# Performance work log

Hardware: AMD Instinct MI355X
Metric: run time of the kernel (lower is better)

Reference implementation:

```python
import jax, jax.numpy as jnp
import numpy as np

D_IN = 256
H = 512


def _linear_params(key, fan_in, fan_out):
    kw, kb = jax.random.split(key)
    bound = 1.0 / np.sqrt(fan_in)
    W = jax.random.uniform(kw, (fan_in, fan_out), minval=-bound, maxval=bound, dtype=jnp.float32)
    b = jax.random.uniform(kb, (fan_out,), minval=-bound, maxval=bound, dtype=jnp.float32)
    return W, b


def setup_inputs() -> dict:
    key = jax.random.key(0)
    ks = jax.random.split(key, 7)
    brick_vectors = jax.random.normal(ks[0], (8, 128, D_IN), dtype=jnp.float32)
    Wa, ba = _linear_params(ks[1], D_IN, H)
    Wb, bb = _linear_params(ks[2], H, H)
    Wca, bca = _linear_params(ks[3], 2 * H, H)
    Wcb, bcb = _linear_params(ks[4], H, H)
    Wcc, bcc = _linear_params(ks[5], H, H)
    Wo, bo = _linear_params(ks[6], H, 2)
    return {
        "brick_vectors": brick_vectors,
        "Wa": Wa, "ba": ba,
        "Wb": Wb, "bb": bb,
        "Wca": Wca, "bca": bca,
        "Wcb": Wcb, "bcb": bcb,
        "Wcc": Wcc, "bcc": bcc,
        "Wo": Wo, "bo": bo,
    }


def reference(brick_vectors, Wa, ba, Wb, bb, Wca, bca, Wcb, bcb, Wcc, bcc, Wo, bo):
    B, N, _ = brick_vectors.shape
    x = brick_vectors.reshape(-1, D_IN)            # [B*N, D_IN]
    f = jax.nn.relu(x @ Wa + ba)                   # node MLP
    f = jax.nn.relu(f @ Wb + bb)                   # [B*N, 512]
    f = f.reshape(B, N, H)
    # pairwise broadcast-concat: pair (i, j) gets cat(f[:, j], f[:, i])
    fa = jnp.broadcast_to(f[:, None, :, :], (B, N, N, H))   # varies over j (last pair axis)
    fb = jnp.broadcast_to(f[:, :, None, :], (B, N, N, H))   # varies over i
    e = jnp.concatenate((fa, fb), axis=-1).reshape(-1, 2 * H)  # [B*N*N, 1024]
    e = jax.nn.relu(e @ Wca + bca)
    e = jax.nn.relu(e @ Wcb + bcb)
    e = jax.nn.relu(e @ Wcc + bcc)
    out = e @ Wo + bo                               # [B*N*N, 2]
    return out.reshape(B, N, N, 2)
```

## Files before the change

kernel.cpp:

```cpp
#include <hip/hip_runtime.h>

typedef __bf16 bf16x8 __attribute__((ext_vector_type(8)));
typedef float f32x16 __attribute__((ext_vector_type(16)));

__global__ __launch_bounds__(256) void prep_pack(const float* __restrict__ Wcb,
                                                 const float* __restrict__ Wcc,
                                                 __bf16* __restrict__ Pb,
                                                 __bf16* __restrict__ Pc) {
  int idx = blockIdx.x * 256 + threadIdx.x;
  const float* src = (idx < 262144) ? Wcb : Wcc;
  __bf16* dst = (idx < 262144) ? Pb : Pc;
  int t = idx & 262143;
  int e = t & 7, l = (t >> 3) & 63, kb = (t >> 9) & 31, c = t >> 14;
  int k = kb * 16 + ((l >> 5) << 3) + e;
  int n = (c << 5) + (l & 31);
  dst[t] = (__bf16)src[k * 512 + n];
}

__global__ __launch_bounds__(256) void gemm_f32(const float* __restrict__ A,
                                                const float* __restrict__ W,
                                                const float* __restrict__ bias,
                                                float* __restrict__ C,
                                                int K, int N, int do_relu) {
  __shared__ float As[16][68];
  __shared__ float Ws[16][32];
  int bm = blockIdx.x * 64, bn = blockIdx.y * 32;
  int tid = threadIdx.x;
  int tx = tid & 15, ty = tid >> 4;
  float acc[4][2] = {};
  for (int k0 = 0; k0 < K; k0 += 16) {
#pragma unroll
    for (int ii = 0; ii < 4; ii++) {
      int e = ii * 256 + tid; int r = e >> 4, c = e & 15;
      As[c][r] = A[(bm + r) * K + k0 + c];
    }
#pragma unroll
    for (int ii = 0; ii < 2; ii++) {
      int e = ii * 256 + tid; int kr = e >> 5, c = e & 31;
      Ws[kr][c] = W[(k0 + kr) * N + bn + c];
    }
    __syncthreads();
#pragma unroll
    for (int kk = 0; kk < 16; kk++) {
      float4 a = *(const float4*)&As[kk][ty * 4];
      float2 w = *(const float2*)&Ws[kk][tx * 2];
      acc[0][0] += a.x * w.x; acc[0][1] += a.x * w.y;
      acc[1][0] += a.y * w.x; acc[1][1] += a.y * w.y;
      acc[2][0] += a.z * w.x; acc[2][1] += a.z * w.y;
      acc[3][0] += a.w * w.x; acc[3][1] += a.w * w.y;
    }
    __syncthreads();
  }
#pragma unroll
  for (int mi = 0; mi < 4; mi++)
#pragma unroll
    for (int ni = 0; ni < 2; ni++) {
      int n = bn + tx * 2 + ni;
      float vv = acc[mi][ni] + (bias ? bias[n] : 0.f);
      if (do_relu) vv = fmaxf(vv, 0.f);
      C[(bm + ty * 4 + mi) * N + n] = vv;
    }
}

__global__ __launch_bounds__(256) void gemm_uv(const float* __restrict__ A,
                                               const float* __restrict__ Wca,
                                               float* __restrict__ u,
                                               float* __restrict__ v) {
  __shared__ float As[16][68];
  __shared__ float Ws[16][32];
  int half = blockIdx.y >> 4;
  const float* W = Wca + half * 512 * 512;
  float* C = half ? v : u;
  int bm = blockIdx.x * 64, bn = (blockIdx.y & 15) * 32;
  int tid = threadIdx.x;
  int tx = tid & 15, ty = tid >> 4;
  float acc[4][2] = {};
  for (int k0 = 0; k0 < 512; k0 += 16) {
#pragma unroll
    for (int ii = 0; ii < 4; ii++) {
      int e = ii * 256 + tid; int r = e >> 4, c = e & 15;
      As[c][r] = A[(bm + r) * 512 + k0 + c];
    }
#pragma unroll
    for (int ii = 0; ii < 2; ii++) {
      int e = ii * 256 + tid; int kr = e >> 5, c = e & 31;
      Ws[kr][c] = W[(k0 + kr) * 512 + bn + c];
    }
    __syncthreads();
#pragma unroll
    for (int kk = 0; kk < 16; kk++) {
      float4 a = *(const float4*)&As[kk][ty * 4];
      float2 w = *(const float2*)&Ws[kk][tx * 2];
      acc[0][0] += a.x * w.x; acc[0][1] += a.x * w.y;
      acc[1][0] += a.y * w.x; acc[1][1] += a.y * w.y;
      acc[2][0] += a.z * w.x; acc[2][1] += a.z * w.y;
      acc[3][0] += a.w * w.x; acc[3][1] += a.w * w.y;
    }
    __syncthreads();
  }
#pragma unroll
  for (int mi = 0; mi < 4; mi++)
#pragma unroll
    for (int ni = 0; ni < 2; ni++)
      C[(bm + ty * 4 + mi) * 512 + bn + tx * 2 + ni] = acc[mi][ni];
}

__global__ __launch_bounds__(512, 2) void edge_kernel(
    const float* __restrict__ u, const float* __restrict__ v,
    const bf16x8* __restrict__ Pb, const bf16x8* __restrict__ Pc,
    const float* __restrict__ bca, const float* __restrict__ bcb,
    const float* __restrict__ bcc, const float* __restrict__ Wo,
    const float* __restrict__ bo, float* __restrict__ out) {
  __shared__ __align__(16) char h_raw[131072];

  int wg = blockIdx.x;
  int i = wg & 127, b = wg >> 7;
  int tid = threadIdx.x, lane = tid & 63, w = tid >> 6;

  int mrow = (w & 1) * 32;
  int n0 = (w >> 1) * 128;
  int cg4 = (w >> 1) * 4;
  int arow = mrow + (lane & 31);
  int sA = (arow & 15) << 4;
  int klo = (lane >> 5) * 8;

  const bf16x8* Bb0 = Pb + ((cg4 + 0) * 32) * 64 + lane;
  const bf16x8* Bb1 = Pb + ((cg4 + 1) * 32) * 64 + lane;
  const bf16x8* Bb2 = Pb + ((cg4 + 2) * 32) * 64 + lane;
  const bf16x8* Bb3 = Pb + ((cg4 + 3) * 32) * 64 + lane;
  const bf16x8* Bc0 = Pc + ((cg4 + 0) * 32) * 64 + lane;
  const bf16x8* Bc1 = Pc + ((cg4 + 1) * 32) * 64 + lane;
  const bf16x8* Bc2 = Pc + ((cg4 + 2) * 32) * 64 + lane;
  const bf16x8* Bc3 = Pc + ((cg4 + 3) * 32) * 64 + lane;

  bf16x8 pf0 = Bb0[0], pf1 = Bb1[0], pf2 = Bb2[0], pf3 = Bb3[0];

  {
    int k2 = tid & 255;
    float2 vv = *(const float2*)(v + (b * 128 + i) * 512 + 2 * k2);
    float2 bc = *(const float2*)(bca + 2 * k2);
    float vb0 = vv.x + bc.x, vb1 = vv.y + bc.y;
    const float* ub = u + (b * 128) * 512;
#pragma unroll 4
    for (int it = 0; it < 64; it++) {
      int r = it * 2 + (tid >> 8);
      float2 uu = *(const float2*)(ub + r * 512 + 2 * k2);
      float x0 = fmaxf(uu.x + vb0, 0.f);
      float x1 = fmaxf(uu.y + vb1, 0.f);
      unsigned short s0 = __builtin_bit_cast(unsigned short, (__bf16)x0);
      unsigned short s1 = __builtin_bit_cast(unsigned short, (__bf16)x1);
      unsigned int pk = ((unsigned int)s1 << 16) | (unsigned int)s0;
      int rt = r & 63;
      int wbyte = ((r >> 6) << 16) + rt * 1024 + ((4 * k2) ^ ((rt & 15) << 4));
      *(unsigned int*)(h_raw + wbyte) = pk;
    }
  }
  __syncthreads();

  f32x16 acc0[4], acc1[4];

#pragma unroll
  for (int nb = 0; nb < 4; nb++)
#pragma unroll
    for (int r = 0; r < 16; r++) { acc0[nb][r] = 0.f; acc1[nb][r] = 0.f; }
#pragma unroll 2
  for (int kb = 0; kb < 32; kb++) {
    bf16x8 b0 = pf0, b1 = pf1, b2 = pf2, b3 = pf3;
    if (kb < 31) {
      pf0 = Bb0[(kb + 1) * 64];
      pf1 = Bb1[(kb + 1) * 64];
      pf2 = Bb2[(kb + 1) * 64];
      pf3 = Bb3[(kb + 1) * 64];
    }
    int abyte = arow * 1024 + (((kb * 16 + klo) * 2) ^ sA);
    bf16x8 a0 = *(const bf16x8*)(h_raw + abyte);
    bf16x8 a1 = *(const bf16x8*)(h_raw + 65536 + abyte);
    acc0[0] = __builtin_amdgcn_mfma_f32_32x32x16_bf16(a0, b0, acc0[0], 0, 0, 0);
    acc1[0] = __builtin_amdgcn_mfma_f32_32x32x16_bf16(a1, b0, acc1[0], 0, 0, 0);
    acc0[1] = __builtin_amdgcn_mfma_f32_32x32x16_bf16(a0, b1, acc0[1], 0, 0, 0);
    acc1[1] = __builtin_amdgcn_mfma_f32_32x32x16_bf16(a1, b1, acc1[1], 0, 0, 0);
    acc0[2] = __builtin_amdgcn_mfma_f32_32x32x16_bf16(a0, b2, acc0[2], 0, 0, 0);
    acc1[2] = __builtin_amdgcn_mfma_f32_32x32x16_bf16(a1, b2, acc1[2], 0, 0, 0);
    acc0[3] = __builtin_amdgcn_mfma_f32_32x32x16_bf16(a0, b3, acc0[3], 0, 0, 0);
    acc1[3] = __builtin_amdgcn_mfma_f32_32x32x16_bf16(a1, b3, acc1[3], 0, 0, 0);
  }

  pf0 = Bc0[0]; pf1 = Bc1[0]; pf2 = Bc2[0]; pf3 = Bc3[0];
  __syncthreads();

#pragma unroll
  for (int nb = 0; nb < 4; nb++) {
    int cn = n0 + nb * 32 + (lane & 31);
    float bbv = bcb[cn];
#pragma unroll
    for (int r = 0; r < 16; r++) {
      int row = mrow + (r & 3) + 8 * (r >> 2) + 4 * (lane >> 5);
      int byte_ = row * 1024 + ((cn * 2) ^ ((row & 15) << 4));
      *(__bf16*)(h_raw + byte_) = (__bf16)fmaxf(acc0[nb][r] + bbv, 0.f);
      *(__bf16*)(h_raw + 65536 + byte_) = (__bf16)fmaxf(acc1[nb][r] + bbv, 0.f);
    }
  }
  __syncthreads();

#pragma unroll
  for (int nb = 0; nb < 4; nb++)
#pragma unroll
    for (int r = 0; r < 16; r++) { acc0[nb][r] = 0.f; acc1[nb][r] = 0.f; }
#pragma unroll 2
  for (int kb = 0; kb < 32; kb++) {
    bf16x8 b0 = pf0, b1 = pf1, b2 = pf2, b3 = pf3;
    if (kb < 31) {
      pf0 = Bc0[(kb + 1) * 64];
      pf1 = Bc1[(kb + 1) * 64];
      pf2 = Bc2[(kb + 1) * 64];
      pf3 = Bc3[(kb + 1) * 64];
    }
    int abyte = arow * 1024 + (((kb * 16 + klo) * 2) ^ sA);
    bf16x8 a0 = *(const bf16x8*)(h_raw + abyte);
    bf16x8 a1 = *(const bf16x8*)(h_raw + 65536 + abyte);
    acc0[0] = __builtin_amdgcn_mfma_f32_32x32x16_bf16(a0, b0, acc0[0], 0, 0, 0);
    acc1[0] = __builtin_amdgcn_mfma_f32_32x32x16_bf16(a1, b0, acc1[0], 0, 0, 0);
    acc0[1] = __builtin_amdgcn_mfma_f32_32x32x16_bf16(a0, b1, acc0[1], 0, 0, 0);
    acc1[1] = __builtin_amdgcn_mfma_f32_32x32x16_bf16(a1, b1, acc1[1], 0, 0, 0);
    acc0[2] = __builtin_amdgcn_mfma_f32_32x32x16_bf16(a0, b2, acc0[2], 0, 0, 0);
    acc1[2] = __builtin_amdgcn_mfma_f32_32x32x16_bf16(a1, b2, acc1[2], 0, 0, 0);
    acc0[3] = __builtin_amdgcn_mfma_f32_32x32x16_bf16(a0, b3, acc0[3], 0, 0, 0);
    acc1[3] = __builtin_amdgcn_mfma_f32_32x32x16_bf16(a1, b3, acc1[3], 0, 0, 0);
  }

  float p0[16][2] = {}, p1[16][2] = {};
#pragma unroll
  for (int nb = 0; nb < 4; nb++) {
    int cn = n0 + nb * 32 + (lane & 31);
    float bcv = bcc[cn];
    float2 wov = *(const float2*)(Wo + cn * 2);
#pragma unroll
    for (int r = 0; r < 16; r++) {
      float h30 = fmaxf(acc0[nb][r] + bcv, 0.f);
      float h31 = fmaxf(acc1[nb][r] + bcv, 0.f);
      p0[r][0] += h30 * wov.x; p0[r][1] += h30 * wov.y;
      p1[r][0] += h31 * wov.x; p1[r][1] += h31 * wov.y;
    }
  }
#pragma unroll
  for (int m = 1; m <= 16; m <<= 1) {
#pragma unroll
    for (int r = 0; r < 16; r++) {
      p0[r][0] += __shfl_xor(p0[r][0], m, 64);
      p0[r][1] += __shfl_xor(p0[r][1], m, 64);
      p1[r][0] += __shfl_xor(p1[r][0], m, 64);
      p1[r][1] += __shfl_xor(p1[r][1], m, 64);
    }
  }
  __syncthreads();
  float* red = (float*)h_raw;
  if ((lane & 31) == 0) {
    int hh = lane >> 5, cg = w >> 1;
#pragma unroll
    for (int r = 0; r < 16; r++) {
      int row = mrow + (r & 3) + 8 * (r >> 2) + 4 * hh;
      red[(cg * 128 + row) * 2 + 0] = p0[r][0];
      red[(cg * 128 + row) * 2 + 1] = p0[r][1];
      red[(cg * 128 + 64 + row) * 2 + 0] = p1[r][0];
      red[(cg * 128 + 64 + row) * 2 + 1] = p1[r][1];
    }
  }
  __syncthreads();
  if (tid < 256) {
    int row = tid >> 1, d = tid & 1;
    float s = red[(0 * 128 + row) * 2 + d] + red[(1 * 128 + row) * 2 + d] +
              red[(2 * 128 + row) * 2 + d] + red[(3 * 128 + row) * 2 + d] + bo[d];
    out[((b * 128 + i) * 128 + row) * 2 + d] = s;
  }
}

extern "C" void kernel_launch(void* const* d_in, const int* in_sizes, int n_in,
                              void* d_out, int out_size, void* d_ws, size_t ws_size,
                              hipStream_t stream) {
  const float* x   = (const float*)d_in[0];
  const float* Wa  = (const float*)d_in[1];
  const float* ba  = (const float*)d_in[2];
  const float* Wb  = (const float*)d_in[3];
  const float* bb  = (const float*)d_in[4];
  const float* Wca = (const float*)d_in[5];
  const float* bca = (const float*)d_in[6];
  const float* Wcb = (const float*)d_in[7];
  const float* bcb = (const float*)d_in[8];
  const float* Wcc = (const float*)d_in[9];
  const float* bcc = (const float*)d_in[10];
  const float* Wo  = (const float*)d_in[11];
  const float* bo  = (const float*)d_in[12];
  float* out = (float*)d_out;

  char* ws = (char*)d_ws;
  float* f1 = (float*)(ws);
  float* f  = (float*)(ws + (2u << 20));
  float* u  = (float*)(ws + (4u << 20));
  float* v  = (float*)(ws + (6u << 20));
  __bf16* Pb = (__bf16*)(ws + (8u << 20));
  __bf16* Pc = (__bf16*)(ws + (8u << 20) + (512u << 10));

  prep_pack<<<2048, 256, 0, stream>>>(Wcb, Wcc, Pb, Pc);
  gemm_f32<<<dim3(16, 16), 256, 0, stream>>>(x, Wa, ba, f1, 256, 512, 1);
  gemm_f32<<<dim3(16, 16), 256, 0, stream>>>(f1, Wb, bb, f, 512, 512, 1);
  gemm_uv<<<dim3(16, 32), 256, 0, stream>>>(f, Wca, u, v);
  edge_kernel<<<1024, 512, 0, stream>>>(u, v, (const bf16x8*)Pb, (const bf16x8*)Pc,
                                        bca, bcb, bcc, Wo, bo, out);
}
```

Before: 255.6 us.

## Stage packed weight tiles into LDS with double-buffered global_load_lds

Previously every wave loaded its own B fragments for the two edge-MLP GEMMs straight from global memory into registers. Wave pairs with different row halves loaded identical data, so each fragment was fetched twice. The new code has each wave fetch two column-blocks of the next k-slice directly into a double-buffered LDS region through the global-to-LDS load path. All waves then read their four fragments from LDS. This removes the duplicated global traffic and the register prefetch, but adds a workgroup barrier on every k-iteration and grows the LDS allocation to 160 KB.

```diff
diff --git a/kernel.cpp b/kernel.cpp
--- a/kernel.cpp
+++ b/kernel.cpp
@@ -2,6 +2,11 @@
 
 typedef __bf16 bf16x8 __attribute__((ext_vector_type(8)));
 typedef float f32x16 __attribute__((ext_vector_type(16)));
+
+#define GLOAD_LDS16(gsrc, ldst)                                                   \
+  __builtin_amdgcn_global_load_lds(                                               \
+      (const __attribute__((address_space(1))) void*)(gsrc),                      \
+      (__attribute__((address_space(3))) void*)(ldst), 16, 0, 0)
 
 __global__ __launch_bounds__(256) void prep_pack(const float* __restrict__ Wcb,
                                                  const float* __restrict__ Wcc,
@@ -111,7 +116,8 @@
     const float* __restrict__ bca, const float* __restrict__ bcb,
     const float* __restrict__ bcc, const float* __restrict__ Wo,
     const float* __restrict__ bo, float* __restrict__ out) {
-  __shared__ __align__(16) char h_raw[131072];
+  __shared__ __align__(16) char h_raw[163840];
+  char* Bst = h_raw + 131072;
 
   int wg = blockIdx.x;
   int i = wg & 127, b = wg >> 7;
@@ -123,17 +129,17 @@
   int arow = mrow + (lane & 31);
   int sA = (arow & 15) << 4;
   int klo = (lane >> 5) * 8;
-
-  const bf16x8* Bb0 = Pb + ((cg4 + 0) * 32) * 64 + lane;
-  const bf16x8* Bb1 = Pb + ((cg4 + 1) * 32) * 64 + lane;
-  const bf16x8* Bb2 = Pb + ((cg4 + 2) * 32) * 64 + lane;
-  const bf16x8* Bb3 = Pb + ((cg4 + 3) * 32) * 64 + lane;
-  const bf16x8* Bc0 = Pc + ((cg4 + 0) * 32) * 64 + lane;
-  const bf16x8* Bc1 = Pc + ((cg4 + 1) * 32) * 64 + lane;
-  const bf16x8* Bc2 = Pc + ((cg4 + 2) * 32) * 64 + lane;
-  const bf16x8* Bc3 = Pc + ((cg4 + 3) * 32) * 64 + lane;
-
-  bf16x8 pf0 = Bb0[0], pf1 = Bb1[0], pf2 = Bb2[0], pf3 = Bb3[0];
+  int cb0 = 2 * w;
+
+#define STAGE_B(P, kb, sel)                                                       \
+  {                                                                               \
+    const char* _g0 = (const char*)((P) + (cb0 * 32 + (kb)) * 64) + lane * 16;    \
+    const char* _g1 = (const char*)((P) + ((cb0 + 1) * 32 + (kb)) * 64) + lane * 16; \
+    GLOAD_LDS16(_g0, Bst + (sel) * 16384 + cb0 * 1024);                           \
+    GLOAD_LDS16(_g1, Bst + (sel) * 16384 + (cb0 + 1) * 1024);                     \
+  }
+
+  STAGE_B(Pb, 0, 0)
 
   {
     int k2 = tid & 255;
@@ -165,13 +171,13 @@
     for (int r = 0; r < 16; r++) { acc0[nb][r] = 0.f; acc1[nb][r] = 0.f; }
 #pragma unroll 2
   for (int kb = 0; kb < 32; kb++) {
-    bf16x8 b0 = pf0, b1 = pf1, b2 = pf2, b3 = pf3;
-    if (kb < 31) {
-      pf0 = Bb0[(kb + 1) * 64];
-      pf1 = Bb1[(kb + 1) * 64];
-      pf2 = Bb2[(kb + 1) * 64];
-      pf3 = Bb3[(kb + 1) * 64];
-    }
+    int sel = kb & 1;
+    if (kb < 31) STAGE_B(Pb, kb + 1, sel ^ 1)
+    const char* bb = Bst + sel * 16384 + lane * 16;
+    bf16x8 b0 = *(const bf16x8*)(bb + (cg4 + 0) * 1024);
+    bf16x8 b1 = *(const bf16x8*)(bb + (cg4 + 1) * 1024);
+    bf16x8 b2 = *(const bf16x8*)(bb + (cg4 + 2) * 1024);
+    bf16x8 b3 = *(const bf16x8*)(bb + (cg4 + 3) * 1024);
     int abyte = arow * 1024 + (((kb * 16 + klo) * 2) ^ sA);
     bf16x8 a0 = *(const bf16x8*)(h_raw + abyte);
     bf16x8 a1 = *(const bf16x8*)(h_raw + 65536 + abyte);
@@ -183,10 +189,9 @@
     acc1[2] = __builtin_amdgcn_mfma_f32_32x32x16_bf16(a1, b2, acc1[2], 0, 0, 0);
     acc0[3] = __builtin_amdgcn_mfma_f32_32x32x16_bf16(a0, b3, acc0[3], 0, 0, 0);
     acc1[3] = __builtin_amdgcn_mfma_f32_32x32x16_bf16(a1, b3, acc1[3], 0, 0, 0);
-  }
-
-  pf0 = Bc0[0]; pf1 = Bc1[0]; pf2 = Bc2[0]; pf3 = Bc3[0];
-  __syncthreads();
+    __syncthreads();
+  }
+  STAGE_B(Pc, 0, 0)
 
 #pragma unroll
   for (int nb = 0; nb < 4; nb++) {
@@ -208,13 +213,13 @@
     for (int r = 0; r < 16; r++) { acc0[nb][r] = 0.f; acc1[nb][r] = 0.f; }
 #pragma unroll 2
   for (int kb = 0; kb < 32; kb++) {
-    bf16x8 b0 = pf0, b1 = pf1, b2 = pf2, b3 = pf3;
-    if (kb < 31) {
-      pf0 = Bc0[(kb + 1) * 64];
-      pf1 = Bc1[(kb + 1) * 64];
-      pf2 = Bc2[(kb + 1) * 64];
-      pf3 = Bc3[(kb + 1) * 64];
-    }
+    int sel = kb & 1;
+    if (kb < 31) STAGE_B(Pc, kb + 1, sel ^ 1)
+    const char* bb = Bst + sel * 16384 + lane * 16;
+    bf16x8 b0 = *(const bf16x8*)(bb + (cg4 + 0) * 1024);
+    bf16x8 b1 = *(const bf16x8*)(bb + (cg4 + 1) * 1024);
+    bf16x8 b2 = *(const bf16x8*)(bb + (cg4 + 2) * 1024);
+    bf16x8 b3 = *(const bf16x8*)(bb + (cg4 + 3) * 1024);
     int abyte = arow * 1024 + (((kb * 16 + klo) * 2) ^ sA);
     bf16x8 a0 = *(const bf16x8*)(h_raw + abyte);
     bf16x8 a1 = *(const bf16x8*)(h_raw + 65536 + abyte);
@@ -226,6 +231,7 @@
     acc1[2] = __builtin_amdgcn_mfma_f32_32x32x16_bf16(a1, b2, acc1[2], 0, 0, 0);
     acc0[3] = __builtin_amdgcn_mfma_f32_32x32x16_bf16(a0, b3, acc0[3], 0, 0, 0);
     acc1[3] = __builtin_amdgcn_mfma_f32_32x32x16_bf16(a1, b3, acc1[3], 0, 0, 0);
+    __syncthreads();
   }
 
   float p0[16][2] = {}, p1[16][2] = {};
@@ -272,6 +278,7 @@
               red[(2 * 128 + row) * 2 + d] + red[(3 * 128 + row) * 2 + d] + bo[d];
     out[((b * 128 + i) * 128 + row) * 2 + d] = s;
   }
+#undef STAGE_B
 }
 
 extern "C" void kernel_launch(void* const* d_in, const int* in_sizes, int n_in,
```

Measured after the change: 255.6 us. Within noise of the previous version (+0.0%).
